# Optimization experiments

Hardware: AMD Instinct MI355X
Metric: run time of the kernel (lower is better)

The kernel has to match this reference:

```python
import jax, jax.numpy as jnp
import numpy as np

Q = 128      # number of slices
S = 8        # slice_length = C // Q = 1024 // 128
H = 32       # unit_dim[0]
BN_EPS = 1e-3  # Keras BatchNormalization default epsilon


def setup_inputs() -> dict:
    key = jax.random.key(0)
    ks = jax.random.split(key, 5)
    B = 32768
    x = jax.random.normal(ks[0], (B, 1, 1, Q * S), dtype=jnp.float32)
    # Per-slice (grouped) parameters for the q=128 independent MLPs.
    W1 = jax.random.normal(ks[1], (Q, S, H), dtype=jnp.float32) / np.sqrt(S)
    b1 = jnp.zeros((Q, H), dtype=jnp.float32)
    gamma = jnp.ones((Q, H), dtype=jnp.float32)
    beta = jnp.zeros((Q, H), dtype=jnp.float32)
    mov_mean = 0.1 * jax.random.normal(ks[2], (Q, H), dtype=jnp.float32)
    mov_var = jnp.ones((Q, H), dtype=jnp.float32) + 0.1 * jax.random.uniform(ks[3], (Q, H), dtype=jnp.float32)
    W2 = jax.random.normal(ks[4], (Q, H, 1), dtype=jnp.float32) / np.sqrt(H)
    b2 = jnp.zeros((Q, 1), dtype=jnp.float32)
    return {"x": x, "W1": W1, "b1": b1, "gamma": gamma, "beta": beta,
            "mov_mean": mov_mean, "mov_var": mov_var, "W2": W2, "b2": b2}


def reference(x, W1, b1, gamma, beta, mov_mean, mov_var, W2, b2):
    B = x.shape[0]
    xs = x.reshape(B, Q, -1)                       # (B, Q, S)
    # Grouped Dense(32) + ELU, all 128 slices in one batched matmul
    h = jnp.einsum('bqs,qsh->bqh', xs, W1) + b1    # (B, Q, H)
    h = jax.nn.elu(h)
    # BatchNormalization (inference: moving statistics)
    inv = gamma * jax.lax.rsqrt(mov_var + BN_EPS)  # (Q, H)
    h = (h - mov_mean) * inv + beta
    # Grouped Dense(1)
    out = jnp.einsum('bqh,qho->bqo', h, W2) + b2   # (B, Q, 1)
    return out[..., 0]                              # (B, Q)
```

## Files before the change

### kernel.cpp

```cpp
#include <hip/hip_runtime.h>
#include <hip/hip_bf16.h>


#define QN 128
#define SN 8
#define HN 32
#define XROW 1024
#define BN_EPS 1e-3f

typedef short bf16x8 __attribute__((ext_vector_type(8)));
typedef float f32x16 __attribute__((ext_vector_type(16)));
typedef unsigned int u32;

#define WS_A_BYTES (QN * 64 * 16)
#define WS_W_OFF   WS_A_BYTES
#define WS_W_BYTES (QN * 32 * 4)
#define WS_B2_OFF  (WS_W_OFF + WS_W_BYTES)

static __device__ __forceinline__ u32 pkbf(float lo, float hi) {
    union { __hip_bfloat162 h2; u32 u; } c;
    c.h2 = __float22bfloat162_rn(float2{lo, hi});
    return c.u;
}
static __device__ __forceinline__ float rfl(float v) {
    return __uint_as_float(__builtin_amdgcn_readfirstlane(__float_as_uint(v)));
}

__global__ void divenc_prep(const float* __restrict__ W1, const float* __restrict__ b1,
                            const float* __restrict__ gamma_, const float* __restrict__ beta_,
                            const float* __restrict__ mmean, const float* __restrict__ mvar,
                            const float* __restrict__ W2, const float* __restrict__ b2,
                            unsigned char* __restrict__ ws)
{
    const int q = blockIdx.x;
    const int m = threadIdx.x;

    u32 d0 = 0, d1 = 0, d2 = 0, d3 = 0;
    if (m < 32) {
        d0 = pkbf(W1[(q*SN + 0)*HN + m], W1[(q*SN + 1)*HN + m]);
        d1 = pkbf(W1[(q*SN + 2)*HN + m], W1[(q*SN + 3)*HN + m]);
        d2 = pkbf(W1[(q*SN + 4)*HN + m], W1[(q*SN + 5)*HN + m]);
        d3 = pkbf(W1[(q*SN + 6)*HN + m], W1[(q*SN + 7)*HN + m]);
    } else {
        d0 = pkbf(b1[q*HN + (m - 32)], 0.f);
    }
    ((uint4*)ws)[q*64 + m] = uint4{d0, d1, d2, d3};

    float* wsW  = (float*)(ws + WS_W_OFF);
    float* wsB2 = (float*)(ws + WS_B2_OFF);
    if (m < 32) {
        const int half = m >> 4, r = m & 15;
        const int h = (r & 3) + 8*(r >> 2) + 4*half;
        float inv = gamma_[q*HN+h] * rsqrtf(mvar[q*HN+h] + BN_EPS);
        wsW[q*32 + m] = inv * W2[q*HN + h];
    }
    if (m == 0) {
        float acc = b2[q];
        for (int h = 0; h < HN; ++h) {
            float inv = gamma_[q*HN+h] * rsqrtf(mvar[q*HN+h] + BN_EPS);
            acc += (beta_[q*HN+h] - mmean[q*HN+h]*inv) * W2[q*HN+h];
        }
        wsB2[q] = acc;
    }
}

__global__ __launch_bounds__(512, 6)
void divenc_mfma(const float* __restrict__ x, const unsigned char* __restrict__ ws,
                 float* __restrict__ out)
{
    const int tid  = threadIdx.x;
    const int lane = tid & 63;
    const int wv   = __builtin_amdgcn_readfirstlane(tid >> 6);
    const int bl   = lane & 31;
    const bool hi  = lane >= 32;
    const int b0   = blockIdx.x * 128;
    const int q0   = blockIdx.y * 32;

    const uint4* wsA  = (const uint4*)ws;
    const float* wsW  = (const float*)(ws + WS_W_OFF);
    const float* wsB2 = (const float*)(ws + WS_B2_OFF);

    __shared__ float slab[128][33];

    #pragma unroll
    for (int qg = 0; qg < 4; ++qg) {
        const int q = q0 + qg*8 + wv;

        union { uint4 u; bf16x8 v; } A;
        A.u = wsA[q*64 + lane];

        const float* wp = wsW + q*32;
        float sw[32];
        #pragma unroll
        for (int r = 0; r < 32; ++r) sw[r] = rfl(wp[r]);
        const float b2p = rfl(wsB2[q]);

        const float* xq = x + (size_t)(b0 + bl) * XROW + q * SN;

        #pragma unroll
        for (int sub = 0; sub < 4; ++sub) {
            const float* xp = xq + (size_t)(sub * 32) * XROW;
            float4 xa = *(const float4*)xp;
            float4 xc = *(const float4*)(xp + 4);

            const u32 k0 = pkbf(xa.x, xa.y), k1 = pkbf(xa.z, xa.w);
            const u32 k2 = pkbf(xc.x, xc.y), k3 = pkbf(xc.z, xc.w);

            union { uint4 u; bf16x8 v; } B;
            B.u = uint4{ hi ? 0x00003F80u : k0,
                         hi ? 0u : k1,
                         hi ? 0u : k2,
                         hi ? 0u : k3 };

            f32x16 Z = {0.f,0.f,0.f,0.f,0.f,0.f,0.f,0.f,
                        0.f,0.f,0.f,0.f,0.f,0.f,0.f,0.f};
            f32x16 D = __builtin_amdgcn_mfma_f32_32x32x16_bf16(A.v, B.v, Z, 0, 0, 0);

            float u_[16];
            #pragma unroll
            for (int r = 0; r < 16; ++r) {
                float z = D[r];
                float e = __expf(fminf(z, 0.f)) - 1.f;
                u_[r] = fmaxf(z, e);
            }
            float p = 0.f;
            if (!hi) {
                #pragma unroll
                for (int r = 0; r < 16; ++r) p = fmaf(u_[r], sw[r], p);
            } else {
                #pragma unroll
                for (int r = 0; r < 16; ++r) p = fmaf(u_[r], sw[16 + r], p);
            }
            p += __shfl_xor(p, 32);
            if (!hi) slab[sub*32 + bl][qg*8 + wv] = p + b2p;
        }
    }

    __syncthreads();

    {
        const int row = tid >> 2;
        const int c0  = (tid & 3) * 8;
        float* orow = out + (size_t)(b0 + row) * QN + q0 + c0;
        float4 v0, v1;
        v0.x = slab[row][c0+0]; v0.y = slab[row][c0+1];
        v0.z = slab[row][c0+2]; v0.w = slab[row][c0+3];
        v1.x = slab[row][c0+4]; v1.y = slab[row][c0+5];
        v1.z = slab[row][c0+6]; v1.w = slab[row][c0+7];
        *(float4*)orow       = v0;
        *(float4*)(orow + 4) = v1;
    }
}

extern "C" void kernel_launch(void* const* d_in, const int* in_sizes, int n_in,
                              void* d_out, int out_size, void* d_ws, size_t ws_size,
                              hipStream_t stream) {
    const float* x      = (const float*)d_in[0];
    const float* W1     = (const float*)d_in[1];
    const float* b1     = (const float*)d_in[2];
    const float* gamma_ = (const float*)d_in[3];
    const float* beta_  = (const float*)d_in[4];
    const float* mmean  = (const float*)d_in[5];
    const float* mvar   = (const float*)d_in[6];
    const float* W2     = (const float*)d_in[7];
    const float* b2     = (const float*)d_in[8];
    float* out = (float*)d_out;
    unsigned char* ws = (unsigned char*)d_ws;

    const int Btot = in_sizes[0] / XROW;

    divenc_prep<<<QN, 64, 0, stream>>>(W1, b1, gamma_, beta_, mmean, mvar, W2, b2, ws);
    divenc_mfma<<<dim3(Btot / 128, QN / 32), 512, 0, stream>>>(x, ws, out);
}
```

Baseline: 55.58 us.

## Split ELU into exp and relu terms, fold -1 into bias, raise occupancy

Rewrites ELU as exp(min(z,0)) + max(z,0) - 1 and folds the constant -1 times the weight into the precomputed output bias, so the epilogue becomes two independent FMA chains without a subtract. The per-q weights are now loaded per lane (each half loads its own 16 values) instead of 32 scalar readfirstlane loads followed by a branch. The q loop is no longer unrolled and uses incremented pointers, and launch bounds are raised to allow 8 blocks per CU. This aims to cut VALU and scalar-load work and register pressure, at the cost of vector loads for the weights and loop overhead.

```diff
diff --git a/kernel.cpp b/kernel.cpp
--- a/kernel.cpp
+++ b/kernel.cpp
@@ -21,9 +21,6 @@
     union { __hip_bfloat162 h2; u32 u; } c;
     c.h2 = __float22bfloat162_rn(float2{lo, hi});
     return c.u;
-}
-static __device__ __forceinline__ float rfl(float v) {
-    return __uint_as_float(__builtin_amdgcn_readfirstlane(__float_as_uint(v)));
 }
 
 __global__ void divenc_prep(const float* __restrict__ W1, const float* __restrict__ b1,
@@ -58,82 +55,77 @@
         float acc = b2[q];
         for (int h = 0; h < HN; ++h) {
             float inv = gamma_[q*HN+h] * rsqrtf(mvar[q*HN+h] + BN_EPS);
-            acc += (beta_[q*HN+h] - mmean[q*HN+h]*inv) * W2[q*HN+h];
+            float w2p = inv * W2[q*HN + h];
+            acc += (beta_[q*HN+h] - mmean[q*HN+h]*inv) * W2[q*HN+h] - w2p;
         }
         wsB2[q] = acc;
     }
 }
 
-__global__ __launch_bounds__(512, 6)
+__global__ __launch_bounds__(512, 8)
 void divenc_mfma(const float* __restrict__ x, const unsigned char* __restrict__ ws,
                  float* __restrict__ out)
 {
     const int tid  = threadIdx.x;
     const int lane = tid & 63;
-    const int wv   = __builtin_amdgcn_readfirstlane(tid >> 6);
+    const int wv   = tid >> 6;
+    const int half = lane >> 5;
     const int bl   = lane & 31;
     const bool hi  = lane >= 32;
     const int b0   = blockIdx.x * 128;
     const int q0   = blockIdx.y * 32;
 
-    const uint4* wsA  = (const uint4*)ws;
-    const float* wsW  = (const float*)(ws + WS_W_OFF);
-    const float* wsB2 = (const float*)(ws + WS_B2_OFF);
-
     __shared__ float slab[128][33];
 
-    #pragma unroll
+    const uint4* wsA  = (const uint4*)ws + (size_t)(q0 + wv) * 64;
+    const float* wsW  = (const float*)(ws + WS_W_OFF) + (q0 + wv) * 32 + half * 16;
+    const float* wsB2 = (const float*)(ws + WS_B2_OFF) + (q0 + wv);
+    const float* xq   = x + (size_t)(b0 + bl) * XROW + (q0 + wv) * SN;
+
+    #pragma unroll 1
     for (int qg = 0; qg < 4; ++qg) {
-        const int q = q0 + qg*8 + wv;
+        union { uint4 u; bf16x8 v; } A;
+        A.u = wsA[lane];
 
-        union { uint4 u; bf16x8 v; } A;
-        A.u = wsA[q*64 + lane];
-
-        const float* wp = wsW + q*32;
-        float sw[32];
+        float w2r[16];
         #pragma unroll
-        for (int r = 0; r < 32; ++r) sw[r] = rfl(wp[r]);
-        const float b2p = rfl(wsB2[q]);
-
-        const float* xq = x + (size_t)(b0 + bl) * XROW + q * SN;
+        for (int r = 0; r < 16; ++r) w2r[r] = wsW[r];
+        const float b2p = wsB2[0];
 
         #pragma unroll
         for (int sub = 0; sub < 4; ++sub) {
             const float* xp = xq + (size_t)(sub * 32) * XROW;
-            float4 xa = *(const float4*)xp;
-            float4 xc = *(const float4*)(xp + 4);
-
-            const u32 k0 = pkbf(xa.x, xa.y), k1 = pkbf(xa.z, xa.w);
-            const u32 k2 = pkbf(xc.x, xc.y), k3 = pkbf(xc.z, xc.w);
+            const float4 xa = *(const float4*)xp;
+            const float4 xc = *(const float4*)(xp + 4);
 
             union { uint4 u; bf16x8 v; } B;
-            B.u = uint4{ hi ? 0x00003F80u : k0,
-                         hi ? 0u : k1,
-                         hi ? 0u : k2,
-                         hi ? 0u : k3 };
+            B.u = uint4{ hi ? 0x00003F80u : pkbf(xa.x, xa.y),
+                         hi ? 0u : pkbf(xa.z, xa.w),
+                         hi ? 0u : pkbf(xc.x, xc.y),
+                         hi ? 0u : pkbf(xc.z, xc.w) };
 
-            f32x16 Z = {0.f,0.f,0.f,0.f,0.f,0.f,0.f,0.f,
-                        0.f,0.f,0.f,0.f,0.f,0.f,0.f,0.f};
+            const f32x16 Z = {0.f,0.f,0.f,0.f,0.f,0.f,0.f,0.f,
+                              0.f,0.f,0.f,0.f,0.f,0.f,0.f,0.f};
             f32x16 D = __builtin_amdgcn_mfma_f32_32x32x16_bf16(A.v, B.v, Z, 0, 0, 0);
 
-            float u_[16];
+            float p0 = 0.f, p1 = 0.f;
             #pragma unroll
             for (int r = 0; r < 16; ++r) {
-                float z = D[r];
-                float e = __expf(fminf(z, 0.f)) - 1.f;
-                u_[r] = fmaxf(z, e);
+                const float z = D[r];
+                const float E = __expf(fminf(z, 0.f));
+                const float R = fmaxf(z, 0.f);
+                p0 = fmaf(E, w2r[r], p0);
+                p1 = fmaf(R, w2r[r], p1);
             }
-            float p = 0.f;
-            if (!hi) {
-                #pragma unroll
-                for (int r = 0; r < 16; ++r) p = fmaf(u_[r], sw[r], p);
-            } else {
-                #pragma unroll
-                for (int r = 0; r < 16; ++r) p = fmaf(u_[r], sw[16 + r], p);
-            }
+            float p = p0 + p1;
             p += __shfl_xor(p, 32);
             if (!hi) slab[sub*32 + bl][qg*8 + wv] = p + b2p;
         }
+
+        wsA  += 8 * 64;
+        wsW  += 8 * 32;
+        wsB2 += 8;
+        xq   += 8 * SN;
     }
 
     __syncthreads();
```

After: 51.87 us. -6.7%, faster.
